# Kernel tuning notes

Measured on AMD Instinct MI355X. Metric: run time of the kernel, lower is better.

Reference implementation:

```python
import jax, jax.numpy as jnp
import numpy as np

N_NODES = 50000
N_EDGES = 400000
IN_F = 512
HID = 512      # 2 * out_features
OUT_F = 256
N_CELL = 1000
N_DIM = 128
N_SEL = 8192
N_C = 1024


def setup_inputs() -> dict:
    key = jax.random.key(0)
    ks = jax.random.split(key, 16)
    x = jax.random.normal(ks[0], (N_NODES, IN_F), dtype=jnp.float32)
    src = jax.random.randint(ks[1], (N_EDGES,), 0, N_NODES, dtype=jnp.int32)
    dst = jax.random.randint(ks[2], (N_EDGES,), 0, N_NODES, dtype=jnp.int32)
    x_indices = jax.random.randint(ks[3], (N_SEL,), 0, N_NODES, dtype=jnp.int32)
    c_indices = jax.random.randint(ks[4], (N_C,), 0, N_CELL, dtype=jnp.int32)
    s = lambda f: 1.0 / np.sqrt(f)
    W1 = jax.random.normal(ks[5], (IN_F, HID), dtype=jnp.float32) * s(IN_F)
    b1 = jnp.zeros((HID,), jnp.float32)
    W2 = jax.random.normal(ks[6], (HID, HID), dtype=jnp.float32) * s(HID)
    b2 = jnp.zeros((HID,), jnp.float32)
    W3 = jax.random.normal(ks[7], (HID, OUT_F), dtype=jnp.float32) * s(HID)
    b3 = jnp.zeros((OUT_F,), jnp.float32)
    Wp = jax.random.normal(ks[8], (OUT_F, N_DIM), dtype=jnp.float32) * s(OUT_F)
    bp = jnp.zeros((N_DIM,), jnp.float32)
    emb = jax.random.normal(ks[9], (N_CELL, N_DIM), dtype=jnp.float32)
    return {"x": x, "src": src, "dst": dst, "x_indices": x_indices,
            "c_indices": c_indices, "W1": W1, "b1": b1, "W2": W2, "b2": b2,
            "W3": W3, "b3": b3, "Wp": Wp, "bp": bp, "emb": emb}


def _degree_norms(src, dst, n):
    ones = jnp.ones(src.shape[0], jnp.float32)
    deg_out = jax.ops.segment_sum(ones, src, num_segments=n)
    deg_in = jax.ops.segment_sum(ones, dst, num_segments=n)
    ns = jnp.where(deg_out > 0, jax.lax.rsqrt(jnp.maximum(deg_out, 1.0)), 0.0)
    nd = jnp.where(deg_in > 0, jax.lax.rsqrt(jnp.maximum(deg_in, 1.0)), 0.0)
    return ns[:, None], nd[:, None]


def _gconv(h, src, dst, norm_src, norm_dst, W, b, n):
    # DGL GraphConv, norm='both': D_in^{-1/2} A D_out^{-1/2} H W + b
    msg = (h * norm_src)[src]                         # [E, F]
    agg = jax.ops.segment_sum(msg, dst, num_segments=n)
    return (agg * norm_dst) @ W + b


def reference(x, src, dst, x_indices, c_indices, W1, b1, W2, b2, W3, b3, Wp, bp, emb):
    n = x.shape[0]
    ns, nd = _degree_norms(src, dst, n)
    h = jax.nn.relu(_gconv(x, src, dst, ns, nd, W1, b1, n))
    h = jax.nn.relu(_gconv(h, src, dst, ns, nd, W2, b2, n))
    h = jax.nn.relu(_gconv(h, src, dst, ns, nd, W3, b3, n))
    enc = h[x_indices]                                # [N_SEL, OUT_F]
    proj = enc @ Wp + bp                              # Dropout in eval mode = identity
    e = emb[c_indices]                                # [N_C, N_DIM]
    return e @ proj.T                                 # [N_C, N_SEL]
```

## Files before the change

kernel.cpp:

```cpp
#include <hip/hip_runtime.h>

typedef unsigned int u32;
typedef unsigned short u16;

#define N_NODES 50000
#define N_EDGES 400000
#define IN_F 512
#define HID 512
#define OUT_F 256
#define N_CELL 1000
#define N_DIM 128
#define N_SEL 8192
#define N_C 1024
#define MPAD 50176

#define SCAN_B 256
#define SCAN_NB ((N_NODES + SCAN_B - 1) / SCAN_B)

typedef __bf16 bf16x8 __attribute__((ext_vector_type(8)));
typedef float f32x4 __attribute__((ext_vector_type(4)));

__device__ __forceinline__ u16 f2bf(float f) {
    u32 u = __builtin_bit_cast(u32, f);
    u32 r = (u + 0x7fffu + ((u >> 16) & 1u)) >> 16;
    return (u16)r;
}
__device__ __forceinline__ float bf2f(u32 bits16) {
    return __builtin_bit_cast(float, bits16 << 16);
}

__device__ __forceinline__ void async_copy16(const u16* g, u16* l) {
    __builtin_amdgcn_global_load_lds(
        (const __attribute__((address_space(1))) void*)g,
        (__attribute__((address_space(3))) void*)l, 16, 0, 0);
}


__global__ void degrees_kernel(const int* __restrict__ src, const int* __restrict__ dst,
                               int* __restrict__ degO, int* __restrict__ degI) {
    int e = blockIdx.x * 256 + threadIdx.x;
    if (e < N_EDGES) {
        atomicAdd(&degO[src[e]], 1);
        atomicAdd(&degI[dst[e]], 1);
    }
}

__global__ void scan_blocksum_kernel(const int* __restrict__ deg, int* __restrict__ bsum) {
    __shared__ int sh[SCAN_B];
    int i = blockIdx.x * SCAN_B + threadIdx.x;
    int v = (i < N_NODES) ? deg[i] : 0;
    sh[threadIdx.x] = v;
    __syncthreads();
    for (int off = SCAN_B / 2; off > 0; off >>= 1) {
        if (threadIdx.x < off) sh[threadIdx.x] += sh[threadIdx.x + off];
        __syncthreads();
    }
    if (threadIdx.x == 0) bsum[blockIdx.x] = sh[0];
}

__global__ void scan_bsum_kernel(const int* __restrict__ bsum, int* __restrict__ boff) {
    __shared__ int sh[SCAN_B];
    const int t = threadIdx.x;
    int v = (t < SCAN_NB) ? bsum[t] : 0;
    sh[t] = v;
    __syncthreads();
    for (int off = 1; off < SCAN_B; off <<= 1) {
        int u = (t >= off) ? sh[t - off] : 0;
        __syncthreads();
        sh[t] += u;
        __syncthreads();
    }
    if (t < SCAN_NB) boff[t] = sh[t] - v;
}

__global__ void scan_final_kernel(const int* __restrict__ deg, const int* __restrict__ degO,
                                  const int* __restrict__ boff, int* __restrict__ offs,
                                  float* __restrict__ ns, float* __restrict__ nd) {
    __shared__ int sh[SCAN_B];
    const int t = threadIdx.x;
    int i = blockIdx.x * SCAN_B + t;
    int v = (i < N_NODES) ? deg[i] : 0;
    sh[t] = v;
    __syncthreads();
    for (int off = 1; off < SCAN_B; off <<= 1) {
        int u = (t >= off) ? sh[t - off] : 0;
        __syncthreads();
        sh[t] += u;
        __syncthreads();
    }
    if (i < N_NODES) {
        offs[i] = boff[blockIdx.x] + sh[t] - v;
        int dO = degO[i];
        ns[i] = dO > 0 ? rsqrtf((float)dO) : 0.f;
        nd[i] = v > 0 ? rsqrtf((float)v) : 0.f;
    }
    if (i == 0) offs[N_NODES] = N_EDGES;
}

__global__ void fill_csr_kernel(const int* __restrict__ src, const int* __restrict__ dst,
                                int* __restrict__ cursor, const int* __restrict__ offs,
                                int* __restrict__ csr) {
    int e = blockIdx.x * 256 + threadIdx.x;
    if (e < N_EDGES) {
        int d = dst[e];
        int slot = atomicAdd(&cursor[d], 1);
        csr[offs[d] + slot] = src[e];
    }
}


#define TRW1 (512 * 512)
#define TRW2 (TRW1 + 512 * 512)
#define TRW3 (TRW2 + 512 * 256)
#define TRWP (TRW3 + 256 * 128)
__global__ void trans_all_kernel(const float* __restrict__ W1, const float* __restrict__ W2,
                                 const float* __restrict__ W3, const float* __restrict__ Wp,
                                 u16* __restrict__ W1T, u16* __restrict__ W2T,
                                 u16* __restrict__ W3T, u16* __restrict__ WpT) {
    int i = blockIdx.x * 256 + threadIdx.x;
    const float* s;
    u16* d;
    int K, N, j;
    if (i < TRW1)      { s = W1; d = W1T; K = 512; N = 512; j = i; }
    else if (i < TRW2) { s = W2; d = W2T; K = 512; N = 512; j = i - TRW1; }
    else if (i < TRW3) { s = W3; d = W3T; K = 512; N = 256; j = i - TRW2; }
    else               { s = Wp; d = WpT; K = 256; N = 128; j = i - TRW3; }
    int n = j / K, k = j % K;
    d[j] = f2bf(s[k * N + n]);
}

__global__ void convert_x_kernel(const float* __restrict__ x, u16* __restrict__ xb) {
    int i = blockIdx.x * 256 + threadIdx.x;
    int base = i * 4;
    int m = base >> 9;
    ushort4 o;
    if (m < N_NODES) {
        float4 v = *(const float4*)(x + base);
        o.x = f2bf(v.x); o.y = f2bf(v.y); o.z = f2bf(v.z); o.w = f2bf(v.w);
    } else {
        o = make_ushort4(0, 0, 0, 0);
    }
    *(ushort4*)(xb + base) = o;
}

__global__ void gather_emb_kernel(const float* __restrict__ emb, const int* __restrict__ cidx,
                                  u16* __restrict__ eb) {
    int c = blockIdx.x, f = threadIdx.x;
    eb[c * N_DIM + f] = f2bf(emb[(size_t)cidx[c] * N_DIM + f]);
}

__global__ __launch_bounds__(256, 2) void gemm_bf16_nt(
    const u16* __restrict__ A, const u16* __restrict__ B,
    const int* __restrict__ aidx,
    u16* __restrict__ Cb, float* __restrict__ Cf,
    const float* __restrict__ scale, int nScale,
    const float* __restrict__ bias,
    int N, int K, int mtiles) {
    __shared__ __align__(16) u16 As[2 * 4096];
    __shared__ __align__(16) u16 Bs[2 * 4096];
    const int t = threadIdx.x;
    const int n0 = blockIdx.y * 128;
    const int l = t & 63, w = t >> 6;
    const int wm = (w >> 1) << 6, wn = (w & 1) << 6;
    const int lr = l & 15, quad = l >> 4;

    const int lrow = l >> 2;
    const int kof = (l & 3) << 3;
    const int r0 = w, r1 = w + 4;
    const u16* gB0 = B + (size_t)(n0 + r0 * 16 + lrow) * K + kof;
    const u16* gB1 = B + (size_t)(n0 + r1 * 16 + lrow) * K + kof;
    u16* lA0 = As + r0 * 512;
    u16* lA1 = As + r1 * 512;
    u16* lB0 = Bs + r0 * 512;
    u16* lB1 = Bs + r1 * 512;
    const int niter = K >> 5;

    for (int mt = 0; mt < mtiles; ++mt) {
        const int m0 = (blockIdx.x * mtiles + mt) * 128;
        int ar0 = m0 + r0 * 16 + lrow;
        int ar1 = m0 + r1 * 16 + lrow;
        if (aidx) { ar0 = aidx[ar0]; ar1 = aidx[ar1]; }
        const u16* gA0 = A + (size_t)ar0 * K + kof;
        const u16* gA1 = A + (size_t)ar1 * K + kof;

        f32x4 acc[4][4] = {};

        async_copy16(gA0, lA0);
        async_copy16(gA1, lA1);
        async_copy16(gB0, lB0);
        async_copy16(gB1, lB1);

        for (int it = 0; it < niter; ++it) {
            const int cur = (it & 1) << 12;
            const int nxt = 4096 - cur;
            __syncthreads();
            if (it + 1 < niter) {
                const int ks = (it + 1) << 5;
                async_copy16(gA0 + ks, lA0 + nxt);
                async_copy16(gA1 + ks, lA1 + nxt);
                async_copy16(gB0 + ks, lB0 + nxt);
                async_copy16(gB1 + ks, lB1 + nxt);
            }
            bf16x8 af[4], bg[4];
#pragma unroll
            for (int i = 0; i < 4; ++i)
                af[i] = *(const bf16x8*)&As[cur + (wm + i * 16 + lr) * 32 + quad * 8];
#pragma unroll
            for (int j = 0; j < 4; ++j)
                bg[j] = *(const bf16x8*)&Bs[cur + (wn + j * 16 + lr) * 32 + quad * 8];
#pragma unroll
            for (int i = 0; i < 4; ++i)
#pragma unroll
                for (int j = 0; j < 4; ++j)
                    acc[i][j] = __builtin_amdgcn_mfma_f32_16x16x32_bf16(af[i], bg[j], acc[i][j], 0, 0, 0);
        }

#pragma unroll
        for (int i = 0; i < 4; ++i) {
            int rbase = m0 + wm + i * 16 + quad * 4;
#pragma unroll
            for (int j = 0; j < 4; ++j) {
                int col = n0 + wn + j * 16 + lr;
                float bv = bias ? bias[col] : 0.f;
#pragma unroll
                for (int r = 0; r < 4; ++r) {
                    int rg = rbase + r;
                    float sc = scale ? (rg < nScale ? scale[rg] : 0.f) : 1.f;
                    float v = acc[i][j][r] * sc + bv;
                    if (Cb) Cb[(size_t)rg * N + col] = f2bf(v);
                    else    Cf[(size_t)rg * N + col] = v;
                }
            }
        }
    }
}

template <int W32>
struct AggVec;
template <> struct AggVec<4> { using T = uint4; };
template <> struct AggVec<2> { using T = uint2; };

template <int F>
__global__ __launch_bounds__(256) void aggregate_kernel(
    const u16* __restrict__ T, const int* __restrict__ csr,
    const int* __restrict__ offs, const float* __restrict__ nd,
    const float* __restrict__ bias, u16* __restrict__ H) {
    constexpr int W32 = F / 128;
    using VT = typename AggVec<W32>::T;
    const int t = threadIdx.x, w = t >> 6, l = t & 63;
    const int node = blockIdx.x * 4 + w;
    u32* __restrict__ Hrow = (u32*)H + (size_t)node * (F / 2) + l * W32;
    if (node >= N_NODES) {
        VT z = {};
        *(VT*)Hrow = z;
        return;
    }
    const int s0 = __builtin_amdgcn_readfirstlane(offs[node]);
    const int s1 = __builtin_amdgcn_readfirstlane(offs[node + 1]);
    const u32* __restrict__ Tb = (const u32*)T + l * W32;

    float acc[4][2 * W32];
#pragma unroll
    for (int c = 0; c < 4; ++c)
#pragma unroll
        for (int j = 0; j < 2 * W32; ++j) acc[c][j] = 0.f;

    int e = s0;
    for (; e + 8 <= s1; e += 8) {
        int si[8];
#pragma unroll
        for (int c = 0; c < 8; ++c) si[c] = csr[e + c];
        VT v[8];
#pragma unroll
        for (int c = 0; c < 8; ++c)
            v[c] = *(const VT*)(Tb + (size_t)si[c] * (F / 2));
#pragma unroll
        for (int c = 0; c < 8; ++c) {
            const u32* vv = (const u32*)&v[c];
#pragma unroll
            for (int j = 0; j < W32; ++j) {
                acc[c & 3][2 * j] += bf2f(vv[j] & 0xffffu);
                acc[c & 3][2 * j + 1] += bf2f(vv[j] >> 16);
            }
        }
    }
    for (; e + 4 <= s1; e += 4) {
        int si[4];
#pragma unroll
        for (int c = 0; c < 4; ++c) si[c] = csr[e + c];
        VT v[4];
#pragma unroll
        for (int c = 0; c < 4; ++c)
            v[c] = *(const VT*)(Tb + (size_t)si[c] * (F / 2));
#pragma unroll
        for (int c = 0; c < 4; ++c) {
            const u32* vv = (const u32*)&v[c];
#pragma unroll
            for (int j = 0; j < W32; ++j) {
                acc[c][2 * j] += bf2f(vv[j] & 0xffffu);
                acc[c][2 * j + 1] += bf2f(vv[j] >> 16);
            }
        }
    }
    for (; e < s1; ++e) {
        int s = csr[e];
        VT v = *(const VT*)(Tb + (size_t)s * (F / 2));
        const u32* vv = (const u32*)&v;
#pragma unroll
        for (int j = 0; j < W32; ++j) {
            acc[0][2 * j] += bf2f(vv[j] & 0xffffu);
            acc[0][2 * j + 1] += bf2f(vv[j] >> 16);
        }
    }

    const float ndv = nd[node];
    u32 ow[W32];
#pragma unroll
    for (int j = 0; j < W32; ++j) {
        float a0 = acc[0][2 * j] + acc[1][2 * j] + acc[2][2 * j] + acc[3][2 * j];
        float a1 = acc[0][2 * j + 1] + acc[1][2 * j + 1] + acc[2][2 * j + 1] + acc[3][2 * j + 1];
        float r0 = fmaxf(fmaf(a0, ndv, bias[l * 2 * W32 + 2 * j]), 0.f);
        float r1 = fmaxf(fmaf(a1, ndv, bias[l * 2 * W32 + 2 * j + 1]), 0.f);
        ow[j] = (u32)f2bf(r0) | ((u32)f2bf(r1) << 16);
    }
    VT o;
    u32* op = (u32*)&o;
#pragma unroll
    for (int j = 0; j < W32; ++j) op[j] = ow[j];
    *(VT*)Hrow = o;
}


extern "C" void kernel_launch(void* const* d_in, const int* in_sizes, int n_in,
                              void* d_out, int out_size, void* d_ws, size_t ws_size,
                              hipStream_t stream) {
    const float* x   = (const float*)d_in[0];
    const int*   src = (const int*)d_in[1];
    const int*   dst = (const int*)d_in[2];
    const int*   xidx= (const int*)d_in[3];
    const int*   cidx= (const int*)d_in[4];
    const float* W1  = (const float*)d_in[5];
    const float* b1  = (const float*)d_in[6];
    const float* W2  = (const float*)d_in[7];
    const float* b2  = (const float*)d_in[8];
    const float* W3  = (const float*)d_in[9];
    const float* b3  = (const float*)d_in[10];
    const float* Wp  = (const float*)d_in[11];
    const float* bp  = (const float*)d_in[12];
    const float* emb = (const float*)d_in[13];
    float* out = (float*)d_out;

    char* p = (char*)d_ws;
    auto alloc = [&](size_t bytes) {
        char* r = p;
        p += (bytes + 255) & ~(size_t)255;
        return r;
    };
    u16* T    = (u16*)alloc((size_t)MPAD * 512 * 2);
    u16* HX   = (u16*)alloc((size_t)MPAD * 512 * 2);
    u16* W1T  = (u16*)alloc((size_t)512 * 512 * 2);
    u16* W2T  = (u16*)alloc((size_t)512 * 512 * 2);
    u16* W3T  = (u16*)alloc((size_t)256 * 512 * 2);
    u16* WpT  = (u16*)alloc((size_t)128 * 256 * 2);
    u16* projb= (u16*)alloc((size_t)N_SEL * N_DIM * 2);
    u16* eb   = (u16*)alloc((size_t)N_C * N_DIM * 2);
    int* degO   = (int*)alloc(N_NODES * 4);
    int* degI   = (int*)alloc(N_NODES * 4);
    int* cursor = (int*)alloc(N_NODES * 4);
    int* offs   = (int*)alloc((N_NODES + 1) * 4);
    float* ns   = (float*)alloc(N_NODES * 4);
    float* nd   = (float*)alloc(N_NODES * 4);
    int* csr    = (int*)alloc(N_EDGES * 4);
    int* bsum   = (int*)alloc(SCAN_NB * 4);
    int* boff   = (int*)alloc(SCAN_NB * 4);
    if ((size_t)(p - (char*)d_ws) > ws_size) return;

    hipMemsetAsync(degO, 0, (size_t)((char*)offs - (char*)degO), stream);
    degrees_kernel<<<(N_EDGES + 255) / 256, 256, 0, stream>>>(src, dst, degO, degI);
    scan_blocksum_kernel<<<SCAN_NB, SCAN_B, 0, stream>>>(degI, bsum);
    scan_bsum_kernel<<<1, SCAN_B, 0, stream>>>(bsum, boff);
    scan_final_kernel<<<SCAN_NB, SCAN_B, 0, stream>>>(degI, degO, boff, offs, ns, nd);
    fill_csr_kernel<<<(N_EDGES + 255) / 256, 256, 0, stream>>>(src, dst, cursor, offs, csr);

    trans_all_kernel<<<TRWP / 256, 256, 0, stream>>>(W1, W2, W3, Wp, W1T, W2T, W3T, WpT);
    convert_x_kernel<<<(MPAD * 512 / 4) / 256, 256, 0, stream>>>(x, HX);
    gather_emb_kernel<<<N_C, N_DIM, 0, stream>>>(emb, cidx, eb);

    gemm_bf16_nt<<<dim3(MPAD / 256, 512 / 128), 256, 0, stream>>>(
        HX, W1T, nullptr, T, nullptr, ns, N_NODES, nullptr, 512, 512, 2);
    aggregate_kernel<512><<<MPAD / 4, 256, 0, stream>>>(T, csr, offs, nd, b1, HX);
    gemm_bf16_nt<<<dim3(MPAD / 256, 512 / 128), 256, 0, stream>>>(
        HX, W2T, nullptr, T, nullptr, ns, N_NODES, nullptr, 512, 512, 2);
    aggregate_kernel<512><<<MPAD / 4, 256, 0, stream>>>(T, csr, offs, nd, b2, HX);
    gemm_bf16_nt<<<dim3(MPAD / 128, 256 / 128), 256, 0, stream>>>(
        HX, W3T, nullptr, T, nullptr, ns, N_NODES, nullptr, 256, 512, 1);
    aggregate_kernel<256><<<MPAD / 4, 256, 0, stream>>>(T, csr, offs, nd, b3, HX);

    gemm_bf16_nt<<<dim3(N_SEL / 128, 1), 256, 0, stream>>>(
        HX, WpT, xidx, projb, nullptr, nullptr, 0, bp, N_DIM, 256, 1);
    gemm_bf16_nt<<<dim3(N_C / 128, N_SEL / 128), 256, 0, stream>>>(
        eb, projb, nullptr, nullptr, out, nullptr, 0, nullptr, N_SEL, N_DIM, 1);
}
```

Baseline: 666.6 us.

## Replace LDS-staged GEMM with direct global-to-register double-buffered loads

The bf16 GEMM no longer stages A/B tiles through shared memory with async global-to-LDS copies and barriers. Each wave now loads its MFMA fragments straight from global memory into registers, double-buffered across k-steps, with no __syncthreads. Multi-tile-per-block looping is also removed, so the first two GEMMs launch twice as many blocks. This removes LDS traffic and barrier stalls, but the two waves sharing a row or column band now each fetch it, doubling global/L2 reads. The fragment loads are 16-byte reads spread across many rows and may coalesce poorly.

```diff
diff --git a/kernel.cpp b/kernel.cpp
--- a/kernel.cpp
+++ b/kernel.cpp
@@ -27,12 +27,6 @@
 }
 __device__ __forceinline__ float bf2f(u32 bits16) {
     return __builtin_bit_cast(float, bits16 << 16);
-}
-
-__device__ __forceinline__ void async_copy16(const u16* g, u16* l) {
-    __builtin_amdgcn_global_load_lds(
-        (const __attribute__((address_space(1))) void*)g,
-        (__attribute__((address_space(3))) void*)l, 16, 0, 0);
 }
 
 
@@ -149,87 +143,79 @@
     eb[c * N_DIM + f] = f2bf(emb[(size_t)cidx[c] * N_DIM + f]);
 }
 
-__global__ __launch_bounds__(256, 2) void gemm_bf16_nt(
+__global__ __launch_bounds__(256, 2) void gemm_wt(
     const u16* __restrict__ A, const u16* __restrict__ B,
     const int* __restrict__ aidx,
     u16* __restrict__ Cb, float* __restrict__ Cf,
     const float* __restrict__ scale, int nScale,
     const float* __restrict__ bias,
-    int N, int K, int mtiles) {
-    __shared__ __align__(16) u16 As[2 * 4096];
-    __shared__ __align__(16) u16 Bs[2 * 4096];
+    int N, int K) {
     const int t = threadIdx.x;
-    const int n0 = blockIdx.y * 128;
+    const int m0 = blockIdx.x * 128, n0 = blockIdx.y * 128;
     const int l = t & 63, w = t >> 6;
     const int wm = (w >> 1) << 6, wn = (w & 1) << 6;
     const int lr = l & 15, quad = l >> 4;
 
-    const int lrow = l >> 2;
-    const int kof = (l & 3) << 3;
-    const int r0 = w, r1 = w + 4;
-    const u16* gB0 = B + (size_t)(n0 + r0 * 16 + lrow) * K + kof;
-    const u16* gB1 = B + (size_t)(n0 + r1 * 16 + lrow) * K + kof;
-    u16* lA0 = As + r0 * 512;
-    u16* lA1 = As + r1 * 512;
-    u16* lB0 = Bs + r0 * 512;
-    u16* lB1 = Bs + r1 * 512;
+    const u16* ga[4];
+    const u16* gb[4];
+#pragma unroll
+    for (int i = 0; i < 4; ++i) {
+        int row = m0 + wm + i * 16 + lr;
+        if (aidx) row = aidx[row];
+        ga[i] = A + (size_t)row * K + quad * 8;
+        gb[i] = B + (size_t)(n0 + wn + i * 16 + lr) * K + quad * 8;
+    }
+
+    f32x4 acc[4][4] = {};
+    bf16x8 a0[4], b0[4], a1[4], b1[4];
+
+#pragma unroll
+    for (int i = 0; i < 4; ++i) { a0[i] = *(const bf16x8*)ga[i]; b0[i] = *(const bf16x8*)gb[i]; }
+
     const int niter = K >> 5;
-
-    for (int mt = 0; mt < mtiles; ++mt) {
-        const int m0 = (blockIdx.x * mtiles + mt) * 128;
-        int ar0 = m0 + r0 * 16 + lrow;
-        int ar1 = m0 + r1 * 16 + lrow;
-        if (aidx) { ar0 = aidx[ar0]; ar1 = aidx[ar1]; }
-        const u16* gA0 = A + (size_t)ar0 * K + kof;
-        const u16* gA1 = A + (size_t)ar1 * K + kof;
-
-        f32x4 acc[4][4] = {};
-
-        async_copy16(gA0, lA0);
-        async_copy16(gA1, lA1);
-        async_copy16(gB0, lB0);
-        async_copy16(gB1, lB1);
-
-        for (int it = 0; it < niter; ++it) {
-            const int cur = (it & 1) << 12;
-            const int nxt = 4096 - cur;
-            __syncthreads();
-            if (it + 1 < niter) {
-                const int ks = (it + 1) << 5;
-                async_copy16(gA0 + ks, lA0 + nxt);
-                async_copy16(gA1 + ks, lA1 + nxt);
-                async_copy16(gB0 + ks, lB0 + nxt);
-                async_copy16(gB1 + ks, lB1 + nxt);
-            }
-            bf16x8 af[4], bg[4];
-#pragma unroll
-            for (int i = 0; i < 4; ++i)
-                af[i] = *(const bf16x8*)&As[cur + (wm + i * 16 + lr) * 32 + quad * 8];
+    for (int it = 0; it < niter; it += 2) {
+        {
+            const int ks = (it + 1) << 5;
+#pragma unroll
+            for (int i = 0; i < 4; ++i) {
+                a1[i] = *(const bf16x8*)(ga[i] + ks);
+                b1[i] = *(const bf16x8*)(gb[i] + ks);
+            }
+        }
+#pragma unroll
+        for (int i = 0; i < 4; ++i)
 #pragma unroll
             for (int j = 0; j < 4; ++j)
-                bg[j] = *(const bf16x8*)&Bs[cur + (wn + j * 16 + lr) * 32 + quad * 8];
-#pragma unroll
-            for (int i = 0; i < 4; ++i)
-#pragma unroll
-                for (int j = 0; j < 4; ++j)
-                    acc[i][j] = __builtin_amdgcn_mfma_f32_16x16x32_bf16(af[i], bg[j], acc[i][j], 0, 0, 0);
-        }
-
-#pragma unroll
-        for (int i = 0; i < 4; ++i) {
-            int rbase = m0 + wm + i * 16 + quad * 4;
-#pragma unroll
-            for (int j = 0; j < 4; ++j) {
-                int col = n0 + wn + j * 16 + lr;
-                float bv = bias ? bias[col] : 0.f;
-#pragma unroll
-                for (int r = 0; r < 4; ++r) {
-                    int rg = rbase + r;
-                    float sc = scale ? (rg < nScale ? scale[rg] : 0.f) : 1.f;
-                    float v = acc[i][j][r] * sc + bv;
-                    if (Cb) Cb[(size_t)rg * N + col] = f2bf(v);
-                    else    Cf[(size_t)rg * N + col] = v;
-                }
+                acc[i][j] = __builtin_amdgcn_mfma_f32_16x16x32_bf16(a0[i], b0[j], acc[i][j], 0, 0, 0);
+        if (it + 2 < niter) {
+            const int ks = (it + 2) << 5;
+#pragma unroll
+            for (int i = 0; i < 4; ++i) {
+                a0[i] = *(const bf16x8*)(ga[i] + ks);
+                b0[i] = *(const bf16x8*)(gb[i] + ks);
+            }
+        }
+#pragma unroll
+        for (int i = 0; i < 4; ++i)
+#pragma unroll
+            for (int j = 0; j < 4; ++j)
+                acc[i][j] = __builtin_amdgcn_mfma_f32_16x16x32_bf16(a1[i], b1[j], acc[i][j], 0, 0, 0);
+    }
+
+#pragma unroll
+    for (int i = 0; i < 4; ++i) {
+        int rbase = m0 + wm + i * 16 + quad * 4;
+#pragma unroll
+        for (int j = 0; j < 4; ++j) {
+            int col = n0 + wn + j * 16 + lr;
+            float bv = bias ? bias[col] : 0.f;
+#pragma unroll
+            for (int r = 0; r < 4; ++r) {
+                int rg = rbase + r;
+                float sc = scale ? (rg < nScale ? scale[rg] : 0.f) : 1.f;
+                float v = acc[i][j][r] * sc + bv;
+                if (Cb) Cb[(size_t)rg * N + col] = f2bf(v);
+                else    Cf[(size_t)rg * N + col] = v;
             }
         }
     }
@@ -386,18 +372,18 @@
     convert_x_kernel<<<(MPAD * 512 / 4) / 256, 256, 0, stream>>>(x, HX);
     gather_emb_kernel<<<N_C, N_DIM, 0, stream>>>(emb, cidx, eb);
 
-    gemm_bf16_nt<<<dim3(MPAD / 256, 512 / 128), 256, 0, stream>>>(
-        HX, W1T, nullptr, T, nullptr, ns, N_NODES, nullptr, 512, 512, 2);
+    gemm_wt<<<dim3(MPAD / 128, 512 / 128), 256, 0, stream>>>(
+        HX, W1T, nullptr, T, nullptr, ns, N_NODES, nullptr, 512, 512);
     aggregate_kernel<512><<<MPAD / 4, 256, 0, stream>>>(T, csr, offs, nd, b1, HX);
-    gemm_bf16_nt<<<dim3(MPAD / 256, 512 / 128), 256, 0, stream>>>(
-        HX, W2T, nullptr, T, nullptr, ns, N_NODES, nullptr, 512, 512, 2);
+    gemm_wt<<<dim3(MPAD / 128, 512 / 128), 256, 0, stream>>>(
+        HX, W2T, nullptr, T, nullptr, ns, N_NODES, nullptr, 512, 512);
     aggregate_kernel<512><<<MPAD / 4, 256, 0, stream>>>(T, csr, offs, nd, b2, HX);
-    gemm_bf16_nt<<<dim3(MPAD / 128, 256 / 128), 256, 0, stream>>>(
-        HX, W3T, nullptr, T, nullptr, ns, N_NODES, nullptr, 256, 512, 1);
+    gemm_wt<<<dim3(MPAD / 128, 256 / 128), 256, 0, stream>>>(
+        HX, W3T, nullptr, T, nullptr, ns, N_NODES, nullptr, 256, 512);
     aggregate_kernel<256><<<MPAD / 4, 256, 0, stream>>>(T, csr, offs, nd, b3, HX);
 
-    gemm_bf16_nt<<<dim3(N_SEL / 128, 1), 256, 0, stream>>>(
-        HX, WpT, xidx, projb, nullptr, nullptr, 0, bp, N_DIM, 256, 1);
-    gemm_bf16_nt<<<dim3(N_C / 128, N_SEL / 128), 256, 0, stream>>>(
-        eb, projb, nullptr, nullptr, out, nullptr, 0, nullptr, N_SEL, N_DIM, 1);
-}
+    gemm_wt<<<dim3(N_SEL / 128, 1), 256, 0, stream>>>(
+        HX, WpT, xidx, projb, nullptr, nullptr, 0, bp, N_DIM, 256);
+    gemm_wt<<<dim3(N_C / 128, N_SEL / 128), 256, 0, stream>>>(
+        eb, projb, nullptr, nullptr, out, nullptr, 0, nullptr, N_SEL, N_DIM);
+}
```

Measured after the change: 776.7 us. 1.17x slower.
